# Kernel tuning notes

Measured on AMD Instinct MI355X. Metric: run time of the kernel, lower is better.

Reference implementation:

```python
import jax, jax.numpy as jnp
import numpy as np

N = 50000        # num nodes
D = 128          # hidden_dim
E = 800000       # num edges (avg_degree = 16)
LN_EPS = 1e-5    # torch LayerNorm default eps


def setup_inputs() -> dict:
    key = jax.random.key(0)
    ks = jax.random.split(key, 8)
    x = jax.random.normal(ks[0], (N, D), dtype=jnp.float32)
    edge_rows = jax.random.randint(ks[1], (E,), 0, N, dtype=jnp.int32)
    edge_cols = jax.random.randint(ks[2], (E,), 0, N, dtype=jnp.int32)
    # Parameters (xavier_uniform for lin1 gain=1.0, lin2 gain=0.5; zero biases)
    lim1 = float(np.sqrt(6.0 / (D + D)))           # gain 1.0
    lim2 = 0.5 * float(np.sqrt(6.0 / (D + D)))     # gain 0.5
    W1 = jax.random.uniform(ks[3], (D, D), minval=-lim1, maxval=lim1, dtype=jnp.float32)
    W2 = jax.random.uniform(ks[4], (D, D), minval=-lim2, maxval=lim2, dtype=jnp.float32)
    b1 = jnp.zeros((D,), dtype=jnp.float32)
    b2 = jnp.zeros((D,), dtype=jnp.float32)
    gamma = jnp.ones((D,), dtype=jnp.float32)      # LayerNorm weight
    beta = jnp.zeros((D,), dtype=jnp.float32)      # LayerNorm bias
    eps = jnp.zeros((), dtype=jnp.float32)         # learnable eps, init 0.0
    return {"x": x, "edge_rows": edge_rows, "edge_cols": edge_cols,
            "W1": W1, "b1": b1, "W2": W2, "b2": b2,
            "gamma": gamma, "beta": beta, "eps": eps}


def layer_norm(x, gamma, beta):
    mu = jnp.mean(x, axis=-1, keepdims=True)
    var = jnp.mean((x - mu) ** 2, axis=-1, keepdims=True)
    return (x - mu) * jax.lax.rsqrt(var + LN_EPS) * gamma + beta


def reference(x, edge_rows, edge_cols, W1, b1, W2, b2, gamma, beta, eps):
    h = layer_norm(x, gamma, beta)                               # [N, D]
    # sparse.mm(adj_t, h): neighbor_sum[i] = sum over edges (i <- j) of h[j]
    neighbor_sum = jax.ops.segment_sum(h[edge_cols], edge_rows, num_segments=N)
    h = (1.0 + eps) * h + neighbor_sum
    h = jax.nn.silu(h @ W1.T + b1)                               # lin1 + SiLU
    h = h @ W2.T + b2                                            # lin2 (dropout p=0 -> identity)
    return x + h
```

## Files before the change

kernel.cpp:

```cpp
#include <hip/hip_runtime.h>
#include <hip/hip_bf16.h>

#define N_NODES 50000
#define DIM 128
#define N_EDGES 800000
#define NBUCKETS 196
#define BINA_EPB 4096
#define NBLKA 196
#define SEGCAP 64
#define BSTRIDE_U32 16384
#define BUCKET_CAP 6144
#define LN_BLOCKS 12500

typedef __bf16 bf16_t;
typedef bf16_t bf16x2 __attribute__((ext_vector_type(2)));
typedef bf16_t bf16x4 __attribute__((ext_vector_type(4)));
typedef bf16_t bf16x8 __attribute__((ext_vector_type(8)));
typedef float f32x4 __attribute__((ext_vector_type(4)));

__device__ __forceinline__ float bf_lo(unsigned int u) {
  return __uint_as_float(u << 16);
}
__device__ __forceinline__ float bf_hi(unsigned int u) {
  return __uint_as_float(u & 0xffff0000u);
}

__global__ __launch_bounds__(256) void k_ln_binA(
    const float* __restrict__ x, const float* __restrict__ gamma,
    const float* __restrict__ beta, bf16_t* __restrict__ h,
    const int* __restrict__ erows, const int* __restrict__ ecols,
    unsigned int* __restrict__ tmp, int* __restrict__ cnt,
    const float* __restrict__ W1, const float* __restrict__ W2,
    bf16_t* __restrict__ W1b, bf16_t* __restrict__ W2b) {
  __shared__ int sh_hist[256];
  __shared__ int sh_cur[256];
  const int t = threadIdx.x;

  if (blockIdx.x < NBLKA) {
    const int blk = blockIdx.x;
    sh_hist[t] = 0;
    __syncthreads();
    const int base = blk * BINA_EPB;
    int bkt[16];
    unsigned int pk[16];
#pragma unroll
    for (int i = 0; i < 16; ++i) {
      const int e = base + i * 256 + t;
      if (e < N_EDGES) {
        const int d = erows[e];
        bkt[i] = d >> 8;
        pk[i] = ((unsigned int)(d & 255) << 16) | (unsigned int)ecols[e];
        atomicAdd(&sh_hist[bkt[i]], 1);
      } else {
        bkt[i] = -1;
      }
    }
    __syncthreads();
    if (t < NBUCKETS) cnt[t * NBLKA + blk] = min(sh_hist[t], SEGCAP);
    sh_cur[t] = 0;
    __syncthreads();
#pragma unroll
    for (int i = 0; i < 16; ++i) {
      if (bkt[i] >= 0) {
        const int pos = atomicAdd(&sh_cur[bkt[i]], 1);
        if (pos < SEGCAP)
          tmp[(size_t)bkt[i] * BSTRIDE_U32 + blk * SEGCAP + pos] = pk[i];
      }
    }
    return;
  }

  if (blockIdx.x < NBLKA + 8) {
    const int wid = blockIdx.x - NBLKA;
    const float* src = (wid < 4) ? W1 : W2;
    bf16_t* dst = (wid < 4) ? W1b : W2b;
    const int off = (wid & 3) * 4096 + t * 16;
#pragma unroll
    for (int k = 0; k < 16; k += 4) {
      const float4 u = *(const float4*)(src + off + k);
      *(bf16x4*)(dst + off + k) =
          (bf16x4){(bf16_t)u.x, (bf16_t)u.y, (bf16_t)u.z, (bf16_t)u.w};
    }
    return;
  }

  const int lane = t & 63;
  const int row  = (blockIdx.x - NBLKA - 8) * 4 + (t >> 6);
  const float2 v = *(const float2*)(x + (size_t)row * DIM + lane * 2);
  float s  = v.x + v.y;
  float ss = v.x * v.x + v.y * v.y;
#pragma unroll
  for (int d = 1; d < 64; d <<= 1) {
    s  += __shfl_xor(s, d);
    ss += __shfl_xor(ss, d);
  }
  const float mu   = s * (1.0f / 128.0f);
  const float var  = ss * (1.0f / 128.0f) - mu * mu;
  const float rstd = rsqrtf(var + 1e-5f);
  const float2 g = *(const float2*)(gamma + lane * 2);
  const float2 b = *(const float2*)(beta + lane * 2);
  const float h0 = (v.x - mu) * rstd * g.x + b.x;
  const float h1 = (v.y - mu) * rstd * g.y + b.y;
  *(bf16x2*)(h + (size_t)row * DIM + lane * 2) = (bf16x2){(bf16_t)h0, (bf16_t)h1};
}

__global__ __launch_bounds__(256) void k_binB(
    const unsigned int* __restrict__ tmp, const int* __restrict__ cnt,
    int* __restrict__ nstart, int* __restrict__ nend,
    unsigned short* __restrict__ sorted) {
  __shared__ unsigned int stage[BUCKET_CAP];
  __shared__ int sh_cnt[256];
  __shared__ int sh_cur[256];
  __shared__ int wsum[4];
  const int b = blockIdx.x, t = threadIdx.x;
  const int lane = t & 63, w = t >> 6;

  const int c = (t < NBLKA) ? cnt[b * NBLKA + t] : 0;
  int v = c;
#pragma unroll
  for (int d = 1; d < 64; d <<= 1) {
    const int n = __shfl_up(v, d);
    if (lane >= d) v += n;
  }
  if (lane == 63) wsum[w] = v;
  __syncthreads();
  int woff = 0;
  for (int k = 0; k < w; ++k) woff += wsum[k];
  const int soff = v + woff - c;
  int total = wsum[0] + wsum[1] + wsum[2] + wsum[3];
  if (total > BUCKET_CAP) total = BUCKET_CAP;

  if (c > 0) {
    const unsigned int* seg = tmp + (size_t)b * BSTRIDE_U32 + t * SEGCAP;
    for (int j = 0; j < c; ++j) {
      const int p = soff + j;
      if (p < BUCKET_CAP) stage[p] = seg[j];
    }
  }
  __syncthreads();

  sh_cnt[t] = 0;
  __syncthreads();
  for (int e = t; e < total; e += 256)
    atomicAdd(&sh_cnt[stage[e] >> 16], 1);
  __syncthreads();

  const int val = sh_cnt[t];
  int v2 = val;
#pragma unroll
  for (int d = 1; d < 64; d <<= 1) {
    const int n = __shfl_up(v2, d);
    if (lane >= d) v2 += n;
  }
  __syncthreads();
  if (lane == 63) wsum[w] = v2;
  __syncthreads();
  int woff2 = 0;
  for (int k = 0; k < w; ++k) woff2 += wsum[k];
  const int rs = b * BUCKET_CAP;
  const int st = rs + v2 + woff2 - val;
  const int nidx = b * 256 + t;
  if (nidx < N_NODES) { nstart[nidx] = st; nend[nidx] = st + val; }
  sh_cur[t] = st;
  __syncthreads();

  for (int e = t; e < total; e += 256) {
    const unsigned int pv = stage[e];
    const int pos = atomicAdd(&sh_cur[pv >> 16], 1);
    sorted[pos] = (unsigned short)(pv & 0xffffu);
  }
}

__global__ __launch_bounds__(256) void k_gm(
    const uint2* __restrict__ h4, const int* __restrict__ nstart,
    const int* __restrict__ nend, const unsigned short* __restrict__ sorted,
    const float* __restrict__ epsp, const float* __restrict__ x,
    const bf16_t* __restrict__ W1b, const float* __restrict__ b1,
    const bf16_t* __restrict__ W2b, const float* __restrict__ b2,
    float* __restrict__ out) {
  __shared__ __attribute__((aligned(16))) bf16_t accL[16 * 136];
  __shared__ __attribute__((aligned(16))) bf16_t interL[16 * 136];
  const int t = threadIdx.x, lane = t & 63, w = t >> 6;
  const int half = lane >> 5, l31 = lane & 31;
  const int nodebase = blockIdx.x * 16;
  const float epv = 1.0f + epsp[0];

  for (int i = 0; i < 4; ++i) {
    const int n = w * 4 + i;
    const int gnode = nodebase + n;
    const int s = nstart[gnode], e = nend[gnode];
    f32x4 a0 = {0.f, 0.f, 0.f, 0.f};
    f32x4 a1 = {0.f, 0.f, 0.f, 0.f};
    f32x4 a2v = {0.f, 0.f, 0.f, 0.f};
    f32x4 a3 = {0.f, 0.f, 0.f, 0.f};
    for (int base = s; base < e; base += 64) {
      const int cnt2 = e - base;
      const int m = cnt2 < 64 ? cnt2 : 64;
      const int myidx = (lane < m) ? (int)sorted[base + lane] : 0;
      for (int j = 0; j < m; j += 8) {
        const int o0 = j + half;
        const int o1 = j + 2 + half;
        const int o2 = j + 4 + half;
        const int o3 = j + 6 + half;
        const int s0 = __shfl(myidx, o0);
        const int s1 = __shfl(myidx, o1);
        const int s2 = __shfl(myidx, o2);
        const int s3 = __shfl(myidx, o3);
        uint2 v0 = h4[(size_t)s0 * 32 + l31];
        uint2 v1 = h4[(size_t)s1 * 32 + l31];
        uint2 v2 = h4[(size_t)s2 * 32 + l31];
        uint2 v3 = h4[(size_t)s3 * 32 + l31];
        if (o0 >= m) { v0.x = 0u; v0.y = 0u; }
        if (o1 >= m) { v1.x = 0u; v1.y = 0u; }
        if (o2 >= m) { v2.x = 0u; v2.y = 0u; }
        if (o3 >= m) { v3.x = 0u; v3.y = 0u; }
        a0[0] += bf_lo(v0.x); a0[1] += bf_hi(v0.x);
        a0[2] += bf_lo(v0.y); a0[3] += bf_hi(v0.y);
        a1[0] += bf_lo(v1.x); a1[1] += bf_hi(v1.x);
        a1[2] += bf_lo(v1.y); a1[3] += bf_hi(v1.y);
        a2v[0] += bf_lo(v2.x); a2v[1] += bf_hi(v2.x);
        a2v[2] += bf_lo(v2.y); a2v[3] += bf_hi(v2.y);
        a3[0] += bf_lo(v3.x); a3[1] += bf_hi(v3.x);
        a3[2] += bf_lo(v3.y); a3[3] += bf_hi(v3.y);
      }
    }
    f32x4 tt = (a0 + a1) + (a2v + a3);
#pragma unroll
    for (int k = 0; k < 4; ++k) tt[k] += __shfl_xor(tt[k], 32);
    if (half == 0) {
      const uint2 hv = h4[(size_t)gnode * 32 + l31];
      tt[0] += bf_lo(hv.x) * epv; tt[1] += bf_hi(hv.x) * epv;
      tt[2] += bf_lo(hv.y) * epv; tt[3] += bf_hi(hv.y) * epv;
      *(bf16x4*)&accL[n * 136 + l31 * 4] =
          (bf16x4){(bf16_t)tt[0], (bf16_t)tt[1], (bf16_t)tt[2], (bf16_t)tt[3]};
    }
  }
  __syncthreads();

  const int l15 = lane & 15, lq = lane >> 4;

  bf16x8 af[4];
#pragma unroll
  for (int ks = 0; ks < 4; ++ks)
    af[ks] = *(const bf16x8*)&accL[l15 * 136 + ks * 32 + lq * 8];

  f32x4 c1[2] = {};
#pragma unroll
  for (int cbh = 0; cbh < 2; ++cbh) {
    const int cb = w * 2 + cbh;
    const bf16_t* wrow = W1b + (size_t)(cb * 16 + l15) * DIM;
#pragma unroll
    for (int ks = 0; ks < 4; ++ks) {
      const bf16x8 bf = *(const bf16x8*)(wrow + ks * 32 + lq * 8);
      c1[cbh] = __builtin_amdgcn_mfma_f32_16x16x32_bf16(af[ks], bf, c1[cbh], 0, 0, 0);
    }
  }

#pragma unroll
  for (int cbh = 0; cbh < 2; ++cbh) {
    const int cb = w * 2 + cbh;
    const float b1v = b1[cb * 16 + l15];
#pragma unroll
    for (int r = 0; r < 4; ++r) {
      float v = c1[cbh][r] + b1v;
      v = v / (1.0f + __expf(-v));
      interL[(lq * 4 + r) * 136 + cb * 16 + l15] = (bf16_t)v;
    }
  }
  __syncthreads();

  bf16x8 a2[4];
#pragma unroll
  for (int ks = 0; ks < 4; ++ks)
    a2[ks] = *(const bf16x8*)&interL[l15 * 136 + ks * 32 + lq * 8];

  f32x4 c2[2] = {};
#pragma unroll
  for (int cbh = 0; cbh < 2; ++cbh) {
    const int cb = w * 2 + cbh;
    const bf16_t* wrow = W2b + (size_t)(cb * 16 + l15) * DIM;
#pragma unroll
    for (int ks = 0; ks < 4; ++ks) {
      const bf16x8 bf = *(const bf16x8*)(wrow + ks * 32 + lq * 8);
      c2[cbh] = __builtin_amdgcn_mfma_f32_16x16x32_bf16(a2[ks], bf, c2[cbh], 0, 0, 0);
    }
  }

#pragma unroll
  for (int cbh = 0; cbh < 2; ++cbh) {
    const int cb = w * 2 + cbh;
    const int c = cb * 16 + l15;
    const float b2v = b2[c];
#pragma unroll
    for (int r = 0; r < 4; ++r) {
      const size_t row = nodebase + lq * 4 + r;
      out[row * DIM + c] = x[row * DIM + c] + c2[cbh][r] + b2v;
    }
  }
}

extern "C" void kernel_launch(void* const* d_in, const int* in_sizes, int n_in,
                              void* d_out, int out_size, void* d_ws, size_t ws_size,
                              hipStream_t stream) {
  const float* x     = (const float*)d_in[0];
  const int*   erows = (const int*)d_in[1];
  const int*   ecols = (const int*)d_in[2];
  const float* W1    = (const float*)d_in[3];
  const float* b1    = (const float*)d_in[4];
  const float* W2    = (const float*)d_in[5];
  const float* b2    = (const float*)d_in[6];
  const float* gamma = (const float*)d_in[7];
  const float* beta  = (const float*)d_in[8];
  const float* eps   = (const float*)d_in[9];
  float* out = (float*)d_out;

  char* ws = (char*)d_ws;
  bf16_t* h         = (bf16_t*)(ws);
  unsigned int* tmp = (unsigned int*)(ws + 12800000);
  int*    cnt       = (int*)(ws + 25645056);
  unsigned short* sorted = (unsigned short*)(ws + 25798720);
  int*    nstart    = (int*)(ws + 28207168);
  int*    nend      = (int*)(ws + 28407168);
  bf16_t* W1b       = (bf16_t*)(ws + 28607168);
  bf16_t* W2b       = (bf16_t*)(ws + 28639936);

  k_ln_binA<<<NBLKA + 8 + LN_BLOCKS, 256, 0, stream>>>(
      x, gamma, beta, h, erows, ecols, tmp, cnt, W1, W2, W1b, W2b);
  k_binB<<<NBUCKETS, 256, 0, stream>>>(tmp, cnt, nstart, nend, sorted);
  k_gm<<<N_NODES / 16, 256, 0, stream>>>(
      (const uint2*)h, nstart, nend, sorted, eps, x, W1b, b1, W2b, b2, out);
}
```

Before: 82.77 us.

## Split bf16 node features into four column planes for cache-local gathers

The LayerNorm output is now stored as four planes of 32 columns each (64 bytes per node per plane) instead of one 256-byte row per node. The gather kernel loops over the planes, so each pass touches a 3.2 MB working set that may stay resident in L2. Each wave now gathers four neighbours per load with 4-byte loads. The cost is four passes over the edge lists and index shuffles, narrower loads, and an extra cross-lane reduction step.

Result: slower. 114.4 us (+38.2%).

```diff
diff --git a/kernel.cpp b/kernel.cpp
--- a/kernel.cpp
+++ b/kernel.cpp
@@ -11,6 +11,7 @@
 #define BSTRIDE_U32 16384
 #define BUCKET_CAP 6144
 #define LN_BLOCKS 12500
+#define PLANE_U32 (N_NODES * 16)
 
 typedef __bf16 bf16_t;
 typedef bf16_t bf16x2 __attribute__((ext_vector_type(2)));
@@ -27,7 +28,7 @@
 
 __global__ __launch_bounds__(256) void k_ln_binA(
     const float* __restrict__ x, const float* __restrict__ gamma,
-    const float* __restrict__ beta, bf16_t* __restrict__ h,
+    const float* __restrict__ beta, bf16_t* __restrict__ hq,
     const int* __restrict__ erows, const int* __restrict__ ecols,
     unsigned int* __restrict__ tmp, int* __restrict__ cnt,
     const float* __restrict__ W1, const float* __restrict__ W2,
@@ -101,7 +102,9 @@
   const float2 b = *(const float2*)(beta + lane * 2);
   const float h0 = (v.x - mu) * rstd * g.x + b.x;
   const float h1 = (v.y - mu) * rstd * g.y + b.y;
-  *(bf16x2*)(h + (size_t)row * DIM + lane * 2) = (bf16x2){(bf16_t)h0, (bf16_t)h1};
+  const int q = lane >> 4, cp = lane & 15;
+  *(bf16x2*)(hq + 2 * ((size_t)q * PLANE_U32 + row * 16 + cp)) =
+      (bf16x2){(bf16_t)h0, (bf16_t)h1};
 }
 
 __global__ __launch_bounds__(256) void k_binB(
@@ -172,7 +175,7 @@
 }
 
 __global__ __launch_bounds__(256) void k_gm(
-    const uint2* __restrict__ h4, const int* __restrict__ nstart,
+    const unsigned int* __restrict__ hq, const int* __restrict__ nstart,
     const int* __restrict__ nend, const unsigned short* __restrict__ sorted,
     const float* __restrict__ epsp, const float* __restrict__ x,
     const bf16_t* __restrict__ W1b, const float* __restrict__ b1,
@@ -181,58 +184,45 @@
   __shared__ __attribute__((aligned(16))) bf16_t accL[16 * 136];
   __shared__ __attribute__((aligned(16))) bf16_t interL[16 * 136];
   const int t = threadIdx.x, lane = t & 63, w = t >> 6;
-  const int half = lane >> 5, l31 = lane & 31;
+  const int es = lane >> 4, cp = lane & 15;
   const int nodebase = blockIdx.x * 16;
   const float epv = 1.0f + epsp[0];
 
-  for (int i = 0; i < 4; ++i) {
-    const int n = w * 4 + i;
-    const int gnode = nodebase + n;
-    const int s = nstart[gnode], e = nend[gnode];
-    f32x4 a0 = {0.f, 0.f, 0.f, 0.f};
-    f32x4 a1 = {0.f, 0.f, 0.f, 0.f};
-    f32x4 a2v = {0.f, 0.f, 0.f, 0.f};
-    f32x4 a3 = {0.f, 0.f, 0.f, 0.f};
-    for (int base = s; base < e; base += 64) {
-      const int cnt2 = e - base;
-      const int m = cnt2 < 64 ? cnt2 : 64;
-      const int myidx = (lane < m) ? (int)sorted[base + lane] : 0;
-      for (int j = 0; j < m; j += 8) {
-        const int o0 = j + half;
-        const int o1 = j + 2 + half;
-        const int o2 = j + 4 + half;
-        const int o3 = j + 6 + half;
-        const int s0 = __shfl(myidx, o0);
-        const int s1 = __shfl(myidx, o1);
-        const int s2 = __shfl(myidx, o2);
-        const int s3 = __shfl(myidx, o3);
-        uint2 v0 = h4[(size_t)s0 * 32 + l31];
-        uint2 v1 = h4[(size_t)s1 * 32 + l31];
-        uint2 v2 = h4[(size_t)s2 * 32 + l31];
-        uint2 v3 = h4[(size_t)s3 * 32 + l31];
-        if (o0 >= m) { v0.x = 0u; v0.y = 0u; }
-        if (o1 >= m) { v1.x = 0u; v1.y = 0u; }
-        if (o2 >= m) { v2.x = 0u; v2.y = 0u; }
-        if (o3 >= m) { v3.x = 0u; v3.y = 0u; }
-        a0[0] += bf_lo(v0.x); a0[1] += bf_hi(v0.x);
-        a0[2] += bf_lo(v0.y); a0[3] += bf_hi(v0.y);
-        a1[0] += bf_lo(v1.x); a1[1] += bf_hi(v1.x);
-        a1[2] += bf_lo(v1.y); a1[3] += bf_hi(v1.y);
-        a2v[0] += bf_lo(v2.x); a2v[1] += bf_hi(v2.x);
-        a2v[2] += bf_lo(v2.y); a2v[3] += bf_hi(v2.y);
-        a3[0] += bf_lo(v3.x); a3[1] += bf_hi(v3.x);
-        a3[2] += bf_lo(v3.y); a3[3] += bf_hi(v3.y);
+#pragma unroll
+  for (int q = 0; q < 4; ++q) {
+    const unsigned int* hp = hq + (size_t)q * PLANE_U32;
+    for (int i = 0; i < 4; ++i) {
+      const int n = w * 4 + i;
+      const int gnode = nodebase + n;
+      const int s = nstart[gnode], e = nend[gnode];
+      float aA0 = 0.f, aA1 = 0.f, aB0 = 0.f, aB1 = 0.f;
+      for (int base = s; base < e; base += 64) {
+        const int cnt2 = e - base;
+        const int m = cnt2 < 64 ? cnt2 : 64;
+        const int myidx = (lane < m) ? (int)sorted[base + lane] : 0;
+        for (int j = 0; j < m; j += 8) {
+          const int o0 = j + es;
+          const int o1 = j + 4 + es;
+          const int s0 = __shfl(myidx, o0);
+          const int s1 = __shfl(myidx, o1);
+          unsigned int v0 = hp[s0 * 16 + cp];
+          unsigned int v1 = hp[s1 * 16 + cp];
+          if (o0 >= m) v0 = 0u;
+          if (o1 >= m) v1 = 0u;
+          aA0 += bf_lo(v0); aA1 += bf_hi(v0);
+          aB0 += bf_lo(v1); aB1 += bf_hi(v1);
+        }
       }
-    }
-    f32x4 tt = (a0 + a1) + (a2v + a3);
-#pragma unroll
-    for (int k = 0; k < 4; ++k) tt[k] += __shfl_xor(tt[k], 32);
-    if (half == 0) {
-      const uint2 hv = h4[(size_t)gnode * 32 + l31];
-      tt[0] += bf_lo(hv.x) * epv; tt[1] += bf_hi(hv.x) * epv;
-      tt[2] += bf_lo(hv.y) * epv; tt[3] += bf_hi(hv.y) * epv;
-      *(bf16x4*)&accL[n * 136 + l31 * 4] =
-          (bf16x4){(bf16_t)tt[0], (bf16_t)tt[1], (bf16_t)tt[2], (bf16_t)tt[3]};
+      float t0 = aA0 + aB0, t1 = aA1 + aB1;
+      t0 += __shfl_xor(t0, 16); t1 += __shfl_xor(t1, 16);
+      t0 += __shfl_xor(t0, 32); t1 += __shfl_xor(t1, 32);
+      if (es == 0) {
+        const unsigned int own = hp[(size_t)gnode * 16 + cp];
+        t0 += bf_lo(own) * epv;
+        t1 += bf_hi(own) * epv;
+        *(bf16x2*)&accL[n * 136 + q * 32 + cp * 2] =
+            (bf16x2){(bf16_t)t0, (bf16_t)t1};
+      }
     }
   }
   __syncthreads();
@@ -315,7 +305,7 @@
   float* out = (float*)d_out;
 
   char* ws = (char*)d_ws;
-  bf16_t* h         = (bf16_t*)(ws);
+  bf16_t* hq        = (bf16_t*)(ws);
   unsigned int* tmp = (unsigned int*)(ws + 12800000);
   int*    cnt       = (int*)(ws + 25645056);
   unsigned short* sorted = (unsigned short*)(ws + 25798720);
@@ -325,8 +315,8 @@
   bf16_t* W2b       = (bf16_t*)(ws + 28639936);
 
   k_ln_binA<<<NBLKA + 8 + LN_BLOCKS, 256, 0, stream>>>(
-      x, gamma, beta, h, erows, ecols, tmp, cnt, W1, W2, W1b, W2b);
+      x, gamma, beta, hq, erows, ecols, tmp, cnt, W1, W2, W1b, W2b);
   k_binB<<<NBUCKETS, 256, 0, stream>>>(tmp, cnt, nstart, nend, sorted);
   k_gm<<<N_NODES / 16, 256, 0, stream>>>(
-      (const uint2*)h, nstart, nend, sorted, eps, x, W1b, b1, W2b, b2, out);
-}
+      (const unsigned int*)hq, nstart, nend, sorted, eps, x, W1b, b1, W2b, b2, out);
+}
```
